# Kernel optimization log

Hardware: AMD Instinct MI355X
Metric: run time of the kernel (lower is better)

The kernel has to match this reference:

```python
import jax, jax.numpy as jnp
import numpy as np
from functools import partial

# ---- constants mirroring init_kwargs ----
T, B, J, I = 1024, 32, 128, 512
KD = 16              # max_delay (dilated kernel size)
THETA = 1.0          # threshold
SIG = 0.5            # delay.SIG, frozen (requires_grad=False)
ALPHA = 5.0          # ATan surrogate alpha
EPS = 1e-5           # BatchNorm eps

# ---- ATan surrogate spike (spikingjelly): fwd = heaviside, bwd = atan grad ----
@jax.custom_vjp
def atan_spike(x):
    return (x >= 0).astype(x.dtype)

def _atan_fwd(x):
    return atan_spike(x), x

def _atan_bwd(x, g):
    return (g * (ALPHA / 2.0) / (1.0 + (jnp.pi / 2.0 * ALPHA * x) ** 2),)

atan_spike.defvjp(_atan_fwd, _atan_bwd)

def _dcls_kernel(w, P):
    # DCLS1d 'gauss' version, kernel_count=1: gaussian bump centered at P + KD//2,
    # normalized over the kernel axis, scaled by weight. w,P: (I,J) -> (I,J,KD)
    c = P + KD // 2
    k = jnp.arange(KD, dtype=w.dtype)                        # (KD,)
    g = jnp.exp(-0.5 * ((k[None, None, :] - c[:, :, None]) / SIG) ** 2)
    g = g / (g.sum(-1, keepdims=True) + 1e-7)
    return w[:, :, None] * g                                  # (I,J,KD)

def setup_inputs() -> dict:
    key = jax.random.key(0)
    ks = jax.random.split(key, 6)
    x = jax.random.normal(ks[0], (T, B, J), dtype=jnp.float32)
    # kaiming_uniform_ fan_in = J*1 -> bound = sqrt(6/fan_in)
    bound = float(np.sqrt(6.0 / J))
    delay_w = jax.random.uniform(ks[1], (I, J), jnp.float32, -bound, bound)
    # P ~ U(-max_delay//2, max_delay//2), then clamped (already in range)
    delay_P = jax.random.uniform(ks[2], (I, J), jnp.float32, -(KD // 2), KD // 2)
    beta = jax.random.uniform(ks[3], (I,), jnp.float32, 0.0, 1.0)
    bn_gamma = jnp.ones((I,), jnp.float32)
    bn_beta = jnp.zeros((I,), jnp.float32)
    U0 = jax.random.uniform(ks[4], (B, I), jnp.float32)       # RandomBatchwiseInit(0,1)
    return {"x": x, "delay_w": delay_w, "delay_P": delay_P, "beta": beta,
            "bn_gamma": bn_gamma, "bn_beta": bn_beta, "U0": U0}

def reference(x, delay_w, delay_P, beta, bn_gamma, bn_beta, U0):
    # --- delayed conv: (T,B,J) -> (B,J,T) -> left-pad KD-1 -> conv1d -> (T,B,I) ---
    xb = jnp.transpose(x, (1, 2, 0))                          # (B,J,T)
    xb = jnp.pad(xb, ((0, 0), (0, 0), (KD - 1, 0)))           # (B,J,T+KD-1)
    kern = _dcls_kernel(delay_w, delay_P)                     # (I,J,KD)
    y = jax.lax.conv_general_dilated(
        xb, kern, window_strides=(1,), padding='VALID',
        dimension_numbers=('NCH', 'OIH', 'NCH'))              # (B,I,T)
    y = jnp.transpose(y, (2, 0, 1))                           # (T,B,I)

    # --- BatchNorm1d over reshaped (T*B, I, 1): stats over T*B per channel ---
    yf = y.reshape(T * B, I)
    mean = yf.mean(axis=0)
    var = yf.var(axis=0)
    yf = (yf - mean) * jax.lax.rsqrt(var + EPS) * bn_gamma + bn_beta
    y = yf.reshape(T, B, I)

    # --- soft-reset LIF scan (NOTE: original passes RAW beta, not sigmoid(beta)) ---
    def step(carry, xt):
        Ut, St = carry
        Ut = beta * (Ut - THETA * St) + (1.0 - beta) * xt
        St = atan_spike(Ut - THETA)
        return (Ut, St), St

    S0 = jnp.zeros_like(U0)
    _, o = jax.lax.scan(step, (U0, S0), y)                    # (T,B,I)
    return o
```

## Files before the change

### kernel.cpp

```cpp
#include <hip/hip_runtime.h>

#define TT 1024
#define NB 32
#define NJ 128
#define NI 512
#define KD 16
#define LVL 1048576

typedef short bf16x8 __attribute__((ext_vector_type(8)));
typedef float floatx4 __attribute__((ext_vector_type(4)));

struct S3 { short h, m, l; };

__device__ __forceinline__ S3 split3(float v) {
    S3 o;
    unsigned hb = __float_as_uint(v) & 0xFFFF0000u;
    float hf = __uint_as_float(hb);
    float r1 = v - hf;
    unsigned mb = __float_as_uint(r1) & 0xFFFF0000u;
    float mf = __uint_as_float(mb);
    float r2 = r1 - mf;
    unsigned lb = __float_as_uint(r2) & 0xFFFF0000u;
    o.h = (short)(hb >> 16);
    o.m = (short)(mb >> 16);
    o.l = (short)(lb >> 16);
    return o;
}

__global__ __launch_bounds__(256) void dcls_kern(const float* __restrict__ w,
                                                 const float* __restrict__ P,
                                                 short* __restrict__ WF) {
    int idx = blockIdx.x * 256 + threadIdx.x;
    int j = idx & (NJ - 1);
    int i = idx >> 7;
    float wv = w[i * NJ + j];
    float c  = P[i * NJ + j] + (float)(KD / 2);
    float g[KD];
    float s = 0.f;
#pragma unroll
    for (int k = 0; k < KD; ++k) {
        float u = (float)k - c;
        g[k] = expf(-2.0f * u * u);
        s += g[k];
    }
    float inv = wv / (s + 1e-7f);
    size_t base = (size_t)(i >> 4) * 32768 + (size_t)(j >> 3) * 128 + (i & 15) * 8 + (j & 7);
#pragma unroll
    for (int d = 0; d < KD; ++d) {
        S3 sp = split3(g[(KD - 1) - d] * inv);
        size_t off = base + (size_t)d * 2048;
        WF[off]           = sp.h;
        WF[off + LVL]     = sp.m;
        WF[off + 2 * LVL] = sp.l;
    }
}

__global__ __launch_bounds__(256, 2) void conv_mfma(const float* __restrict__ x,
                                                    const short* __restrict__ WF,
                                                    float* __restrict__ y) {
    __shared__ __align__(16) short PA[128][64];
    __shared__ __align__(16) short PL[128][64];

    const int t0 = blockIdx.x * 128;
    const int i0 = blockIdx.y * 128;
    const int b  = blockIdx.z;
    const int tid = threadIdx.x;

    const int ch   = tid & 3;
    const int rw2  = tid >> 2;
    const int l    = tid & 63;
    const int wid  = tid >> 6;
    const int lr16 = l & 15;
    const int kb   = l >> 4;
    const int wm   = wid >> 1;
    const int wn   = wid & 1;

    const short* pnf[4];
#pragma unroll
    for (int nf = 0; nf < 4; ++nf) {
        int ig = (i0 + wn * 64 + nf * 16) >> 4;
        pnf[nf] = WF + (size_t)ig * 32768 + l * 8;
    }

    floatx4 acc[4][4];
#pragma unroll
    for (int mf = 0; mf < 4; ++mf)
#pragma unroll
        for (int nf = 0; nf < 4; ++nf)
#pragma unroll
            for (int e = 0; e < 4; ++e) acc[mf][nf][e] = 0.f;

    float4 ga[2][2];
    bf16x8 W0h[4], W0m[4], W0l[4], W1h[4], W1m[4], W1l[4];

#define LOADW(K, H, M, L_) {                                                    \
    int koff = ((((K) >> 2) * 16 + ((K) & 3) * 4)) * 128;                       \
    _Pragma("unroll") for (int nf = 0; nf < 4; ++nf) {                          \
        const short* p = pnf[nf] + koff;                                        \
        H[nf]  = *(const bf16x8*)(p);                                           \
        M[nf]  = *(const bf16x8*)(p + LVL);                                     \
        L_[nf] = *(const bf16x8*)(p + 2 * LVL); } }

#define STEP(K, CH, CM, CL, NH, NM, NL) {                                       \
    __syncthreads();                                                            \
    _Pragma("unroll") for (int s = 0; s < 2; ++s) {                             \
        int r = rw2 + s * 64;                                                   \
        int key = r & 7;                                                        \
        char* rowA = (char*)PA + r * 128;                                       \
        char* rowL = (char*)PL + r * 128;                                       \
        S3 a0 = split3(ga[s][0].x), a1 = split3(ga[s][0].y),                    \
           a2 = split3(ga[s][0].z), a3 = split3(ga[s][0].w),                    \
           a4 = split3(ga[s][1].x), a5 = split3(ga[s][1].y),                    \
           a6 = split3(ga[s][1].z), a7 = split3(ga[s][1].w);                    \
        bf16x8 h8, m8, l8;                                                      \
        h8[0]=a0.h; h8[1]=a1.h; h8[2]=a2.h; h8[3]=a3.h;                         \
        h8[4]=a4.h; h8[5]=a5.h; h8[6]=a6.h; h8[7]=a7.h;                         \
        m8[0]=a0.m; m8[1]=a1.m; m8[2]=a2.m; m8[3]=a3.m;                         \
        m8[4]=a4.m; m8[5]=a5.m; m8[6]=a6.m; m8[7]=a7.m;                         \
        l8[0]=a0.l; l8[1]=a1.l; l8[2]=a2.l; l8[3]=a3.l;                         \
        l8[4]=a4.l; l8[5]=a5.l; l8[6]=a6.l; l8[7]=a7.l;                         \
        *(bf16x8*)(rowA + ((ch ^ key) * 16))       = h8;                        \
        *(bf16x8*)(rowA + (((ch + 4) ^ key) * 16)) = m8;                        \
        *(bf16x8*)(rowL + ((ch ^ key) * 16))       = l8; }                      \
    __syncthreads();                                                            \
    if ((K) + 1 < 64) {                                                         \
        int kn = (K) + 1, dn = kn >> 2, j0n = (kn & 3) << 5;                    \
        _Pragma("unroll") for (int s = 0; s < 2; ++s) {                         \
            int r = rw2 + s * 64;                                               \
            int t = t0 + r - dn;                                                \
            float4 z4 = make_float4(0.f, 0.f, 0.f, 0.f);                        \
            ga[s][0] = z4; ga[s][1] = z4;                                       \
            if (t >= 0) {                                                       \
                const float* ax = x + ((size_t)t * NB + b) * NJ + j0n + ch * 8; \
                ga[s][0] = *(const float4*)ax;                                  \
                ga[s][1] = *(const float4*)(ax + 4); } }                        \
        LOADW(kn, NH, NM, NL) }                                                 \
    _Pragma("unroll") for (int mf = 0; mf < 4; ++mf) {                          \
        int row = wm * 64 + mf * 16 + lr16;                                     \
        int key = row & 7;                                                      \
        const char* rowA = (const char*)PA + row * 128;                         \
        const char* rowL = (const char*)PL + row * 128;                         \
        bf16x8 ah = *(const bf16x8*)(rowA + ((kb ^ key) * 16));                 \
        bf16x8 am = *(const bf16x8*)(rowA + (((kb + 4) ^ key) * 16));           \
        bf16x8 al = *(const bf16x8*)(rowL + ((kb ^ key) * 16));                 \
        _Pragma("unroll") for (int nf = 0; nf < 4; ++nf)                        \
            acc[mf][nf] = __builtin_amdgcn_mfma_f32_16x16x32_bf16(ah, CH[nf], acc[mf][nf], 0, 0, 0); \
        _Pragma("unroll") for (int nf = 0; nf < 4; ++nf)                        \
            acc[mf][nf] = __builtin_amdgcn_mfma_f32_16x16x32_bf16(ah, CM[nf], acc[mf][nf], 0, 0, 0); \
        _Pragma("unroll") for (int nf = 0; nf < 4; ++nf)                        \
            acc[mf][nf] = __builtin_amdgcn_mfma_f32_16x16x32_bf16(am, CH[nf], acc[mf][nf], 0, 0, 0); \
        _Pragma("unroll") for (int nf = 0; nf < 4; ++nf)                        \
            acc[mf][nf] = __builtin_amdgcn_mfma_f32_16x16x32_bf16(am, CM[nf], acc[mf][nf], 0, 0, 0); \
        _Pragma("unroll") for (int nf = 0; nf < 4; ++nf)                        \
            acc[mf][nf] = __builtin_amdgcn_mfma_f32_16x16x32_bf16(ah, CL[nf], acc[mf][nf], 0, 0, 0); \
        _Pragma("unroll") for (int nf = 0; nf < 4; ++nf)                        \
            acc[mf][nf] = __builtin_amdgcn_mfma_f32_16x16x32_bf16(al, CH[nf], acc[mf][nf], 0, 0, 0); \
    } }

#pragma unroll
    for (int s = 0; s < 2; ++s) {
        int r = rw2 + s * 64;
        int t = t0 + r;
        const float* ax = x + ((size_t)t * NB + b) * NJ + ch * 8;
        ga[s][0] = *(const float4*)ax;
        ga[s][1] = *(const float4*)(ax + 4);
    }
    LOADW(0, W0h, W0m, W0l)

#pragma unroll 1
    for (int kk = 0; kk < 64; kk += 2) {
        STEP(kk,     W0h, W0m, W0l, W1h, W1m, W1l)
        STEP(kk + 1, W1h, W1m, W1l, W0h, W0m, W0l)
    }
#undef LOADW
#undef STEP

#pragma unroll
    for (int mf = 0; mf < 4; ++mf)
#pragma unroll
        for (int nf = 0; nf < 4; ++nf) {
            int ic = i0 + wn * 64 + nf * 16 + lr16;
#pragma unroll
            for (int q = 0; q < 4; ++q) {
                int t = t0 + wm * 64 + mf * 16 + kb * 4 + q;
                y[((size_t)t * NB + b) * NI + ic] = acc[mf][nf][q];
            }
        }
}

__global__ __launch_bounds__(256) void red1(const float* __restrict__ y,
                                            float* __restrict__ part) {
    int r0 = blockIdx.x * 128;
    int c  = threadIdx.x;
    float s0 = 0.f, q0 = 0.f, s1 = 0.f, q1 = 0.f;
#pragma unroll 4
    for (int r = 0; r < 128; ++r) {
        float v0 = y[(size_t)(r0 + r) * NI + c];
        float v1 = y[(size_t)(r0 + r) * NI + c + 256];
        s0 += v0; q0 = fmaf(v0, v0, q0);
        s1 += v1; q1 = fmaf(v1, v1, q1);
    }
    part[blockIdx.x * NI + c]            = s0;
    part[blockIdx.x * NI + c + 256]      = s1;
    part[256 * NI + blockIdx.x * NI + c]       = q0;
    part[256 * NI + blockIdx.x * NI + c + 256] = q1;
}

__global__ __launch_bounds__(512) void red2(const float* __restrict__ part,
                                            const float* __restrict__ gamma,
                                            const float* __restrict__ bbeta,
                                            float* __restrict__ sb) {
    int c = threadIdx.x;
    double s = 0.0, q = 0.0;
#pragma unroll 8
    for (int p = 0; p < 256; ++p) {
        s += (double)part[p * NI + c];
        q += (double)part[256 * NI + p * NI + c];
    }
    double mean = s / 32768.0;
    double var  = q / 32768.0 - mean * mean;
    double scale = (double)gamma[c] / sqrt(var + 1e-5);
    sb[c]      = (float)scale;
    sb[NI + c] = (float)((double)bbeta[c] - mean * scale);
}

__global__ __launch_bounds__(64) void scan_kern(float* __restrict__ y,
                                                const float* __restrict__ sb,
                                                const float* __restrict__ beta,
                                                const float* __restrict__ U0) {
    int g = blockIdx.x * 64 + threadIdx.x;
    int i = g & (NI - 1);
    float scale = sb[i];
    float bias  = sb[NI + i];
    float bet = beta[i];
    float omb = 1.f - bet;
    float u = U0[g];
    float s = 0.f;
    float* yp = y + g;

    float A[32], Bv[32];
#pragma unroll
    for (int r = 0; r < 32; ++r) A[r] = yp[(size_t)r * 16384];

    for (int t0 = 0; t0 < TT; t0 += 64) {
#pragma unroll
        for (int r = 0; r < 32; ++r) Bv[r] = yp[(size_t)(t0 + 32 + r) * 16384];
#pragma unroll
        for (int r = 0; r < 32; ++r) {
            float z = fmaf(A[r], scale, bias);
            u = fmaf(bet, u - s, omb * z);
            s = (u >= 1.f) ? 1.f : 0.f;
            yp[(size_t)(t0 + r) * 16384] = s;
        }
        if (t0 + 64 < TT) {
#pragma unroll
            for (int r = 0; r < 32; ++r) A[r] = yp[(size_t)(t0 + 64 + r) * 16384];
        }
#pragma unroll
        for (int r = 0; r < 32; ++r) {
            float z = fmaf(Bv[r], scale, bias);
            u = fmaf(bet, u - s, omb * z);
            s = (u >= 1.f) ? 1.f : 0.f;
            yp[(size_t)(t0 + 32 + r) * 16384] = s;
        }
    }
}

extern "C" void kernel_launch(void* const* d_in, const int* in_sizes, int n_in,
                              void* d_out, int out_size, void* d_ws, size_t ws_size,
                              hipStream_t stream) {
    const float* x       = (const float*)d_in[0];
    const float* delay_w = (const float*)d_in[1];
    const float* delay_P = (const float*)d_in[2];
    const float* beta    = (const float*)d_in[3];
    const float* bn_g    = (const float*)d_in[4];
    const float* bn_b    = (const float*)d_in[5];
    const float* U0      = (const float*)d_in[6];
    float* y = (float*)d_out;

    short* WF   = (short*)d_ws;
    float* part = (float*)d_ws;
    float* sb   = (float*)d_ws + 2 * 256 * NI;

    dcls_kern<<<dim3(NI * NJ / 256), dim3(256), 0, stream>>>(delay_w, delay_P, WF);
    conv_mfma<<<dim3(TT / 128, NI / 128, NB), dim3(256), 0, stream>>>(x, WF, y);
    red1<<<dim3(TT * NB / 128), dim3(256), 0, stream>>>(y, part);
    red2<<<dim3(1), dim3(512), 0, stream>>>(part, bn_g, bn_b, sb);
    scan_kern<<<dim3(NB * NI / 64), dim3(64), 0, stream>>>(y, sb, beta, U0);
}
```

Baseline: 367.8 us.

## Pre-split x into bf16 triples in a separate pass before the MFMA conv

Adds a kernel that splits the fp32 input x once into three bf16 planes (high/mid/low) stored in workspace. A new conv kernel then loads those bf16 planes directly instead of reading fp32 x and splitting it inside every tile, and it requests three blocks per CU instead of two. This removes the repeated split arithmetic across the I-tiles, at the cost of an extra pass over x and a larger workspace. The new path only runs when the workspace is big enough; otherwise it falls back to the old kernel.

```diff
diff --git a/kernel.cpp b/kernel.cpp
--- a/kernel.cpp
+++ b/kernel.cpp
@@ -6,6 +6,7 @@
 #define NI 512
 #define KD 16
 #define LVL 1048576
+#define XLVL 4194304
 
 typedef short bf16x8 __attribute__((ext_vector_type(8)));
 typedef float floatx4 __attribute__((ext_vector_type(4)));
@@ -53,6 +54,140 @@
         WF[off + LVL]     = sp.m;
         WF[off + 2 * LVL] = sp.l;
     }
+}
+
+__global__ __launch_bounds__(256) void xsplit_kern(const float* __restrict__ x,
+                                                   short* __restrict__ XF) {
+    size_t e0 = ((size_t)blockIdx.x * 256 + threadIdx.x) * 8;
+    float4 v0 = *(const float4*)(x + e0);
+    float4 v1 = *(const float4*)(x + e0 + 4);
+    S3 a0 = split3(v0.x), a1 = split3(v0.y), a2 = split3(v0.z), a3 = split3(v0.w);
+    S3 a4 = split3(v1.x), a5 = split3(v1.y), a6 = split3(v1.z), a7 = split3(v1.w);
+    bf16x8 h8, m8, l8;
+    h8[0]=a0.h; h8[1]=a1.h; h8[2]=a2.h; h8[3]=a3.h; h8[4]=a4.h; h8[5]=a5.h; h8[6]=a6.h; h8[7]=a7.h;
+    m8[0]=a0.m; m8[1]=a1.m; m8[2]=a2.m; m8[3]=a3.m; m8[4]=a4.m; m8[5]=a5.m; m8[6]=a6.m; m8[7]=a7.m;
+    l8[0]=a0.l; l8[1]=a1.l; l8[2]=a2.l; l8[3]=a3.l; l8[4]=a4.l; l8[5]=a5.l; l8[6]=a6.l; l8[7]=a7.l;
+    *(bf16x8*)(XF + e0)            = h8;
+    *(bf16x8*)(XF + XLVL + e0)     = m8;
+    *(bf16x8*)(XF + 2 * XLVL + e0) = l8;
+}
+
+__global__ __launch_bounds__(256, 3) void conv_mfma_xf(const short* __restrict__ XF,
+                                                       const short* __restrict__ WF,
+                                                       float* __restrict__ y) {
+    __shared__ __align__(16) short PA[128][64];
+    __shared__ __align__(16) short PL[128][64];
+
+    const int t0 = blockIdx.x * 128;
+    const int i0 = blockIdx.y * 128;
+    const int b  = blockIdx.z;
+    const int tid = threadIdx.x;
+
+    const int ch   = tid & 3;
+    const int rw2  = tid >> 2;
+    const int l    = tid & 63;
+    const int wid  = tid >> 6;
+    const int lr16 = l & 15;
+    const int kb   = l >> 4;
+    const int wm   = wid >> 1;
+    const int wn   = wid & 1;
+
+    const short* pnf[4];
+#pragma unroll
+    for (int nf = 0; nf < 4; ++nf) {
+        int ig = (i0 + wn * 64 + nf * 16) >> 4;
+        pnf[nf] = WF + (size_t)ig * 32768 + l * 8;
+    }
+
+    floatx4 acc[4][4];
+#pragma unroll
+    for (int mf = 0; mf < 4; ++mf)
+#pragma unroll
+        for (int nf = 0; nf < 4; ++nf)
+#pragma unroll
+            for (int e = 0; e < 4; ++e) acc[mf][nf][e] = 0.f;
+
+    bf16x8 xh[2], xm[2], xl[2];
+    bf16x8 W0h[4], W0m[4], W0l[4], W1h[4], W1m[4], W1l[4];
+
+#define LOADW(K, H, M, L_) {                                                    \
+    int koff = ((((K) >> 2) * 16 + ((K) & 3) * 4)) * 128;                       \
+    _Pragma("unroll") for (int nf = 0; nf < 4; ++nf) {                          \
+        const short* p = pnf[nf] + koff;                                        \
+        H[nf]  = *(const bf16x8*)(p);                                           \
+        M[nf]  = *(const bf16x8*)(p + LVL);                                     \
+        L_[nf] = *(const bf16x8*)(p + 2 * LVL); } }
+
+#define LOADX(K) {                                                              \
+    int dn = (K) >> 2, j0n = ((K) & 3) << 5;                                    \
+    _Pragma("unroll") for (int s = 0; s < 2; ++s) {                             \
+        int r = rw2 + s * 64;                                                   \
+        int t = t0 + r - dn;                                                    \
+        bf16x8 z8 = (bf16x8)(short)0;                                           \
+        xh[s] = z8; xm[s] = z8; xl[s] = z8;                                     \
+        if (t >= 0) {                                                           \
+            const short* xp = XF + ((size_t)t * NB + b) * NJ + j0n + ch * 8;    \
+            xh[s] = *(const bf16x8*)(xp);                                       \
+            xm[s] = *(const bf16x8*)(xp + XLVL);                                \
+            xl[s] = *(const bf16x8*)(xp + 2 * XLVL); } } }
+
+#define STEP(K, CH, CM, CL, NH, NM, NL) {                                       \
+    __syncthreads();                                                            \
+    _Pragma("unroll") for (int s = 0; s < 2; ++s) {                             \
+        int r = rw2 + s * 64;                                                   \
+        int key = r & 7;                                                        \
+        char* rowA = (char*)PA + r * 128;                                       \
+        char* rowL = (char*)PL + r * 128;                                       \
+        *(bf16x8*)(rowA + ((ch ^ key) * 16))       = xh[s];                     \
+        *(bf16x8*)(rowA + (((ch + 4) ^ key) * 16)) = xm[s];                     \
+        *(bf16x8*)(rowL + ((ch ^ key) * 16))       = xl[s]; }                   \
+    __syncthreads();                                                            \
+    if ((K) + 1 < 64) { LOADX((K) + 1) LOADW((K) + 1, NH, NM, NL) }             \
+    _Pragma("unroll") for (int mf = 0; mf < 4; ++mf) {                          \
+        int row = wm * 64 + mf * 16 + lr16;                                     \
+        int key = row & 7;                                                      \
+        const char* rowA = (const char*)PA + row * 128;                         \
+        const char* rowL = (const char*)PL + row * 128;                         \
+        bf16x8 ah = *(const bf16x8*)(rowA + ((kb ^ key) * 16));                 \
+        bf16x8 am = *(const bf16x8*)(rowA + (((kb + 4) ^ key) * 16));           \
+        bf16x8 al = *(const bf16x8*)(rowL + ((kb ^ key) * 16));                 \
+        _Pragma("unroll") for (int nf = 0; nf < 4; ++nf)                        \
+            acc[mf][nf] = __builtin_amdgcn_mfma_f32_16x16x32_bf16(ah, CH[nf], acc[mf][nf], 0, 0, 0); \
+        _Pragma("unroll") for (int nf = 0; nf < 4; ++nf)                        \
+            acc[mf][nf] = __builtin_amdgcn_mfma_f32_16x16x32_bf16(ah, CM[nf], acc[mf][nf], 0, 0, 0); \
+        _Pragma("unroll") for (int nf = 0; nf < 4; ++nf)                        \
+            acc[mf][nf] = __builtin_amdgcn_mfma_f32_16x16x32_bf16(am, CH[nf], acc[mf][nf], 0, 0, 0); \
+        _Pragma("unroll") for (int nf = 0; nf < 4; ++nf)                        \
+            acc[mf][nf] = __builtin_amdgcn_mfma_f32_16x16x32_bf16(am, CM[nf], acc[mf][nf], 0, 0, 0); \
+        _Pragma("unroll") for (int nf = 0; nf < 4; ++nf)                        \
+            acc[mf][nf] = __builtin_amdgcn_mfma_f32_16x16x32_bf16(ah, CL[nf], acc[mf][nf], 0, 0, 0); \
+        _Pragma("unroll") for (int nf = 0; nf < 4; ++nf)                        \
+            acc[mf][nf] = __builtin_amdgcn_mfma_f32_16x16x32_bf16(al, CH[nf], acc[mf][nf], 0, 0, 0); \
+    } }
+
+    LOADX(0)
+    LOADW(0, W0h, W0m, W0l)
+
+#pragma unroll 1
+    for (int kk = 0; kk < 64; kk += 2) {
+        STEP(kk,     W0h, W0m, W0l, W1h, W1m, W1l)
+        STEP(kk + 1, W1h, W1m, W1l, W0h, W0m, W0l)
+    }
+#undef LOADW
+#undef LOADX
+#undef STEP
+
+#pragma unroll
+    for (int mf = 0; mf < 4; ++mf)
+#pragma unroll
+        for (int nf = 0; nf < 4; ++nf) {
+            int ic = i0 + wn * 64 + nf * 16 + lr16;
+#pragma unroll
+            for (int q = 0; q < 4; ++q) {
+                int t = t0 + wm * 64 + mf * 16 + kb * 4 + q;
+                y[((size_t)t * NB + b) * NI + ic] = acc[mf][nf][q];
+            }
+        }
 }
 
 __global__ __launch_bounds__(256, 2) void conv_mfma(const float* __restrict__ x,
@@ -279,11 +414,19 @@
     float* y = (float*)d_out;
 
     short* WF   = (short*)d_ws;
+    short* XF   = WF + 3 * (size_t)LVL;
     float* part = (float*)d_ws;
     float* sb   = (float*)d_ws + 2 * 256 * NI;
 
+    const bool use_xf = ws_size >= (size_t)(3 * LVL + 3 * XLVL) * sizeof(short);
+
     dcls_kern<<<dim3(NI * NJ / 256), dim3(256), 0, stream>>>(delay_w, delay_P, WF);
-    conv_mfma<<<dim3(TT / 128, NI / 128, NB), dim3(256), 0, stream>>>(x, WF, y);
+    if (use_xf) {
+        xsplit_kern<<<dim3(TT * NB * NJ / (256 * 8)), dim3(256), 0, stream>>>(x, XF);
+        conv_mfma_xf<<<dim3(TT / 128, NI / 128, NB), dim3(256), 0, stream>>>(XF, WF, y);
+    } else {
+        conv_mfma<<<dim3(TT / 128, NI / 128, NB), dim3(256), 0, stream>>>(x, WF, y);
+    }
     red1<<<dim3(TT * NB / 128), dim3(256), 0, stream>>>(y, part);
     red2<<<dim3(1), dim3(512), 0, stream>>>(part, bn_g, bn_b, sb);
     scan_kern<<<dim3(NB * NI / 64), dim3(64), 0, stream>>>(y, sb, beta, U0);
```

Result: slower. 1.069 ms (+190.8%).

## Double-buffer LDS staging in conv MFMA loop to halve barriers

Applied to the files above, without the earlier changes.

Uses two LDS buffers for the split bf16 activation tiles. The next k-step is staged into the alternate buffer while MFMAs run on the current one, which leaves one barrier per step instead of two. Global loads of x run two steps ahead. LDS use doubles to 64KB per block, which may reduce occupancy under launch_bounds(256,2) and raises register pressure.

```diff
diff --git a/kernel.cpp b/kernel.cpp
--- a/kernel.cpp
+++ b/kernel.cpp
@@ -58,8 +58,8 @@
 __global__ __launch_bounds__(256, 2) void conv_mfma(const float* __restrict__ x,
                                                     const short* __restrict__ WF,
                                                     float* __restrict__ y) {
-    __shared__ __align__(16) short PA[128][64];
-    __shared__ __align__(16) short PL[128][64];
+    __shared__ __align__(16) short PA[2][128][64];
+    __shared__ __align__(16) short PL[2][128][64];
 
     const int t0 = blockIdx.x * 128;
     const int i0 = blockIdx.y * 128;
@@ -101,13 +101,24 @@
         M[nf]  = *(const bf16x8*)(p + LVL);                                     \
         L_[nf] = *(const bf16x8*)(p + 2 * LVL); } }
 
-#define STEP(K, CH, CM, CL, NH, NM, NL) {                                       \
-    __syncthreads();                                                            \
+#define LOADX(K) {                                                              \
+    int dn = (K) >> 2, j0n = ((K) & 3) << 5;                                    \
+    _Pragma("unroll") for (int s = 0; s < 2; ++s) {                             \
+        int r = rw2 + s * 64;                                                   \
+        int t = t0 + r - dn;                                                    \
+        float4 z4 = make_float4(0.f, 0.f, 0.f, 0.f);                            \
+        ga[s][0] = z4; ga[s][1] = z4;                                           \
+        if (t >= 0) {                                                           \
+            const float* ax = x + ((size_t)t * NB + b) * NJ + j0n + ch * 8;     \
+            ga[s][0] = *(const float4*)ax;                                      \
+            ga[s][1] = *(const float4*)(ax + 4); } } }
+
+#define STAGEW(BUFA, BUFL) {                                                    \
     _Pragma("unroll") for (int s = 0; s < 2; ++s) {                             \
         int r = rw2 + s * 64;                                                   \
         int key = r & 7;                                                        \
-        char* rowA = (char*)PA + r * 128;                                       \
-        char* rowL = (char*)PL + r * 128;                                       \
+        char* rowA = (char*)(BUFA) + r * 128;                                   \
+        char* rowL = (char*)(BUFL) + r * 128;                                   \
         S3 a0 = split3(ga[s][0].x), a1 = split3(ga[s][0].y),                    \
            a2 = split3(ga[s][0].z), a3 = split3(ga[s][0].w),                    \
            a4 = split3(ga[s][1].x), a5 = split3(ga[s][1].y),                    \
@@ -121,25 +132,14 @@
         l8[4]=a4.l; l8[5]=a5.l; l8[6]=a6.l; l8[7]=a7.l;                         \
         *(bf16x8*)(rowA + ((ch ^ key) * 16))       = h8;                        \
         *(bf16x8*)(rowA + (((ch + 4) ^ key) * 16)) = m8;                        \
-        *(bf16x8*)(rowL + ((ch ^ key) * 16))       = l8; }                      \
-    __syncthreads();                                                            \
-    if ((K) + 1 < 64) {                                                         \
-        int kn = (K) + 1, dn = kn >> 2, j0n = (kn & 3) << 5;                    \
-        _Pragma("unroll") for (int s = 0; s < 2; ++s) {                         \
-            int r = rw2 + s * 64;                                               \
-            int t = t0 + r - dn;                                                \
-            float4 z4 = make_float4(0.f, 0.f, 0.f, 0.f);                        \
-            ga[s][0] = z4; ga[s][1] = z4;                                       \
-            if (t >= 0) {                                                       \
-                const float* ax = x + ((size_t)t * NB + b) * NJ + j0n + ch * 8; \
-                ga[s][0] = *(const float4*)ax;                                  \
-                ga[s][1] = *(const float4*)(ax + 4); } }                        \
-        LOADW(kn, NH, NM, NL) }                                                 \
+        *(bf16x8*)(rowL + ((ch ^ key) * 16))       = l8; } }
+
+#define DOMFMA(BUFA, BUFL, CH, CM, CL) {                                        \
     _Pragma("unroll") for (int mf = 0; mf < 4; ++mf) {                          \
         int row = wm * 64 + mf * 16 + lr16;                                     \
         int key = row & 7;                                                      \
-        const char* rowA = (const char*)PA + row * 128;                         \
-        const char* rowL = (const char*)PL + row * 128;                         \
+        const char* rowA = (const char*)(BUFA) + row * 128;                     \
+        const char* rowL = (const char*)(BUFL) + row * 128;                     \
         bf16x8 ah = *(const bf16x8*)(rowA + ((kb ^ key) * 16));                 \
         bf16x8 am = *(const bf16x8*)(rowA + (((kb + 4) ^ key) * 16));           \
         bf16x8 al = *(const bf16x8*)(rowL + ((kb ^ key) * 16));                 \
@@ -157,23 +157,29 @@
             acc[mf][nf] = __builtin_amdgcn_mfma_f32_16x16x32_bf16(al, CH[nf], acc[mf][nf], 0, 0, 0); \
     } }
 
-#pragma unroll
-    for (int s = 0; s < 2; ++s) {
-        int r = rw2 + s * 64;
-        int t = t0 + r;
-        const float* ax = x + ((size_t)t * NB + b) * NJ + ch * 8;
-        ga[s][0] = *(const float4*)ax;
-        ga[s][1] = *(const float4*)(ax + 4);
-    }
+    LOADX(0)
+    STAGEW(PA[0], PL[0])
+    LOADX(1)
     LOADW(0, W0h, W0m, W0l)
+    __syncthreads();
 
 #pragma unroll 1
     for (int kk = 0; kk < 64; kk += 2) {
-        STEP(kk,     W0h, W0m, W0l, W1h, W1m, W1l)
-        STEP(kk + 1, W1h, W1m, W1l, W0h, W0m, W0l)
+        if (kk + 1 < 64) { STAGEW(PA[1], PL[1]) }
+        if (kk + 2 < 64) { LOADX(kk + 2) }
+        if (kk + 1 < 64) { LOADW(kk + 1, W1h, W1m, W1l) }
+        DOMFMA(PA[0], PL[0], W0h, W0m, W0l)
+        __syncthreads();
+        if (kk + 2 < 64) { STAGEW(PA[0], PL[0]) }
+        if (kk + 3 < 64) { LOADX(kk + 3) }
+        if (kk + 2 < 64) { LOADW(kk + 2, W0h, W0m, W0l) }
+        if (kk + 1 < 64) { DOMFMA(PA[1], PL[1], W1h, W1m, W1l) }
+        __syncthreads();
     }
 #undef LOADW
-#undef STEP
+#undef LOADX
+#undef STAGEW
+#undef DOMFMA
 
 #pragma unroll
     for (int mf = 0; mf < 4; ++mf)
```

Result: no change. 368.6 us (+0.2%).
